# Kernel optimization log

Hardware: AMD Instinct MI355X
Metric: run time of the kernel (lower is better)

## Reference

```python
import jax, jax.numpy as jnp
import numpy as np

NUM_HEADS = 16
EPS = 1e-6
NEG_INF = -1e9


def layer_norm(x, scale, bias):
    m = jnp.mean(x, axis=-1, keepdims=True)
    v = jnp.mean(jnp.square(x - m), axis=-1, keepdims=True)
    return (x - m) * jax.lax.rsqrt(v + EPS) * scale + bias


def mha(x_q, x_kv, wq, wk, wv, wo, causal):
    B, Sq, D = x_q.shape
    Sk = x_kv.shape[1]
    H = NUM_HEADS
    Dh = D // H
    q = (x_q @ wq).reshape(B, Sq, H, Dh) * (1.0 / np.sqrt(Dh))
    k = (x_kv @ wk).reshape(B, Sk, H, Dh)
    v = (x_kv @ wv).reshape(B, Sk, H, Dh)
    scores = jnp.einsum('bqhf,bkhf->bhqk', q, k)  # [B,H,Sq,Sk]
    if causal:
        mask = jnp.tril(jnp.ones((Sq, Sk), dtype=bool))
        scores = jnp.where(mask, scores, NEG_INF)
    p = jax.nn.softmax(scores, axis=-1)
    o = jnp.einsum('bhqk,bkhf->bqhf', p, v).reshape(B, Sq, D)
    return o @ wo


def setup_inputs() -> dict:
    key = jax.random.key(0)
    ks = jax.random.split(key, 12)
    B, S, D, F = 2, 2048, 1024, 4096
    w = 0.02
    return {
        'targets': jax.random.normal(ks[0], (B, S, D), jnp.float32),
        'encoded': jax.random.normal(ks[1], (B, S, D), jnp.float32),
        'ln1_s': jnp.ones((D,), jnp.float32),
        'ln1_b': jnp.zeros((D,), jnp.float32),
        'sa_wq': jax.random.normal(ks[2], (D, D), jnp.float32) * w,
        'sa_wk': jax.random.normal(ks[3], (D, D), jnp.float32) * w,
        'sa_wv': jax.random.normal(ks[4], (D, D), jnp.float32) * w,
        'sa_wo': jax.random.normal(ks[5], (D, D), jnp.float32) * w,
        'ln2_s': jnp.ones((D,), jnp.float32),
        'ln2_b': jnp.zeros((D,), jnp.float32),
        'ca_wq': jax.random.normal(ks[6], (D, D), jnp.float32) * w,
        'ca_wk': jax.random.normal(ks[7], (D, D), jnp.float32) * w,
        'ca_wv': jax.random.normal(ks[8], (D, D), jnp.float32) * w,
        'ca_wo': jax.random.normal(ks[9], (D, D), jnp.float32) * w,
        'ln3_s': jnp.ones((D,), jnp.float32),
        'ln3_b': jnp.zeros((D,), jnp.float32),
        'mlp_w1': jax.random.normal(ks[10], (D, F), jnp.float32) * w,
        'mlp_b1': jnp.zeros((F,), jnp.float32),
        'mlp_w2': jax.random.normal(ks[11], (F, D), jnp.float32) * w,
        'mlp_b2': jnp.zeros((D,), jnp.float32),
    }


def reference(targets, encoded, ln1_s, ln1_b, sa_wq, sa_wk, sa_wv, sa_wo,
              ln2_s, ln2_b, ca_wq, ca_wk, ca_wv, ca_wo,
              ln3_s, ln3_b, mlp_w1, mlp_b1, mlp_w2, mlp_b2):
    # Pre-LN causal self-attention + residual
    x = layer_norm(targets, ln1_s, ln1_b)
    x = mha(x, x, sa_wq, sa_wk, sa_wv, sa_wo, causal=True)
    x = x + targets
    # Pre-LN cross-attention over encoder output + residual
    y = layer_norm(x, ln2_s, ln2_b)
    y = mha(y, encoded, ca_wq, ca_wk, ca_wv, ca_wo, causal=False)
    y = y + x
    # Pre-LN MLP + residual
    z = layer_norm(y, ln3_s, ln3_b)
    z = jax.nn.relu(z @ mlp_w1 + mlp_b1) @ mlp_w2 + mlp_b2
    return y + z
```

## Files before the change

kernel.cpp:

```cpp
#include <hip/hip_runtime.h>


#define DEV __device__ __forceinline__

typedef __attribute__((ext_vector_type(8))) _Float16 half8;
typedef __attribute__((ext_vector_type(4))) _Float16 half4;
typedef __attribute__((ext_vector_type(2))) _Float16 half2v;
typedef __attribute__((ext_vector_type(4))) float    f32x4;
typedef __attribute__((ext_vector_type(4))) unsigned int uint4v;

#define GLB(p) ((const __attribute__((address_space(1))) void*)(p))
#define LDS(p) ((__attribute__((address_space(3))) void*)(p))

DEV half2v pk(float a, float b) {
  return __builtin_bit_cast(half2v, __builtin_amdgcn_cvt_pkrtz(a, b));
}
DEV half4 pk4(float a, float b, float c, float d) {
  half2v lo = pk(a, b), hi = pk(c, d);
  half4 r; r.x = lo.x; r.y = lo.y; r.z = hi.x; r.w = hi.y;
  return r;
}

DEV float wave_sum_f(float v) {
  #pragma unroll
  for (int off = 32; off; off >>= 1) v += __shfl_xor(v, off);
  return v;
}

struct WtArgs { const float* w[8]; _Float16* wt[8]; };

__global__ __launch_bounds__(256) void wt_square(WtArgs a) {
  const float* w = a.w[blockIdx.z];
  _Float16* wt = a.wt[blockIdx.z];
  __shared__ float t[32][33];
  const int tx = threadIdx.x, ty = threadIdx.y;
  const int n0 = blockIdx.x * 32, k0 = blockIdx.y * 32;
  #pragma unroll
  for (int i = ty; i < 32; i += 8)
    t[i][tx] = w[(size_t)(k0 + i) * 1024 + n0 + tx];
  __syncthreads();
  #pragma unroll
  for (int i = ty; i < 32; i += 8)
    wt[(size_t)(n0 + i) * 1024 + k0 + tx] = (_Float16)t[tx][i];
}

__global__ __launch_bounds__(256) void wt_one(const float* __restrict__ w,
                                              _Float16* __restrict__ wt,
                                              int K, int N) {
  __shared__ float t[32][33];
  const int tx = threadIdx.x, ty = threadIdx.y;
  const int n0 = blockIdx.x * 32, k0 = blockIdx.y * 32;
  #pragma unroll
  for (int i = ty; i < 32; i += 8)
    t[i][tx] = w[(size_t)(k0 + i) * N + n0 + tx];
  __syncthreads();
  #pragma unroll
  for (int i = ty; i < 32; i += 8)
    wt[(size_t)(n0 + i) * K + k0 + tx] = (_Float16)t[tx][i];
}

__global__ __launch_bounds__(256) void cvt_f16(const float* __restrict__ in,
                                               _Float16* __restrict__ out) {
  const size_t i = ((size_t)blockIdx.x * 256 + threadIdx.x) * 4;
  const float4 v = *(const float4*)(in + i);
  *(half4*)(out + i) = pk4(v.x, v.y, v.z, v.w);
}

__global__ __launch_bounds__(256) void ln_kernel(const float* __restrict__ x,
                                                 const float* __restrict__ sc,
                                                 const float* __restrict__ bi,
                                                 _Float16* __restrict__ out) {
  const int row = blockIdx.x;
  const int t = threadIdx.x;
  const float4 v = ((const float4*)(x + (size_t)row * 1024))[t];
  float s  = v.x + v.y + v.z + v.w;
  float s2 = v.x * v.x + v.y * v.y + v.z * v.z + v.w * v.w;
  s = wave_sum_f(s); s2 = wave_sum_f(s2);
  __shared__ float red[8];
  const int lane = t & 63, wid = t >> 6;
  if (lane == 0) { red[wid] = s; red[4 + wid] = s2; }
  __syncthreads();
  s  = red[0] + red[1] + red[2] + red[3];
  s2 = red[4] + red[5] + red[6] + red[7];
  const float mean = s * (1.f / 1024.f);
  const float rstd = rsqrtf(s2 * (1.f / 1024.f) - mean * mean + 1e-6f);
  const float4 sv = ((const float4*)sc)[t];
  const float4 bv = ((const float4*)bi)[t];
  half4 o = pk4((v.x - mean) * rstd * sv.x + bv.x,
                (v.y - mean) * rstd * sv.y + bv.y,
                (v.z - mean) * rstd * sv.z + bv.z,
                (v.w - mean) * rstd * sv.w + bv.w);
  ((half4*)(out + (size_t)row * 1024))[t] = o;
}

template <int EPI, int BM, int BN, int BK>
__global__ __launch_bounds__(256)
void gemm_f16(const _Float16* __restrict__ A, const _Float16* __restrict__ Bt,
              void* __restrict__ Cout, const float* __restrict__ bias,
              const float* __restrict__ resid, int M, int N, int K,
              float scl, int sclCols, _Float16* __restrict__ vt, int vcol0) {
  constexpr int AM = BM / 32;
  constexpr int AN = BN / 32;
  constexpr int RA = BM * BK / 2048;
  constexpr int RB = BN * BK / 2048;
  constexpr int TPR = BK / 8;
  constexpr int RPR = 2048 / BK;
  constexpr int SWM = TPR - 1;
  constexpr int SH  = (TPR == 4) ? 1 : 0;
  __shared__ _Float16 As[2][BM * BK];
  __shared__ _Float16 Bs[2][BN * BK];
  const int tid = threadIdx.x;
  const int lane = tid & 63, wid = tid >> 6;
  const int wm = wid >> 1, wn = wid & 1;
  const int q = lane >> 4, m15 = lane & 15;

  const int nwg = gridDim.x * gridDim.y;
  const int bflat = blockIdx.x + gridDim.x * blockIdx.y;
  const int swz = (bflat & 7) * (nwg >> 3) + (bflat >> 3);
  const int bn = swz % gridDim.x;
  const int bm = swz / gridDim.x;

  const int trow = tid / TPR;
  const int tcolsw = ((tid % TPR) ^ ((trow >> SH) & SWM)) * 8;
  const _Float16* Ab = A + ((size_t)bm * BM + trow) * K + tcolsw;
  const _Float16* Bb = Bt + ((size_t)bn * BN + trow) * K + tcolsw;

  f32x4 acc[AM][AN] = {};

  auto stage = [&](int k0, int buf) {
    #pragma unroll
    for (int r = 0; r < RA; r++)
      __builtin_amdgcn_global_load_lds(GLB(Ab + (size_t)r * RPR * K + k0),
                                       LDS(&As[buf][r * 2048 + wid * 512]), 16, 0, 0);
    #pragma unroll
    for (int r = 0; r < RB; r++)
      __builtin_amdgcn_global_load_lds(GLB(Bb + (size_t)r * RPR * K + k0),
                                       LDS(&Bs[buf][r * 2048 + wid * 512]), 16, 0, 0);
  };

  stage(0, 0);
  const int nit = K / BK;
  for (int it = 0; it < nit; it++) {
    const int buf = it & 1;
    __syncthreads();
    if (it + 1 < nit) stage((it + 1) * BK, buf ^ 1);
    #pragma unroll
    for (int kk = 0; kk < BK / 32; kk++) {
      half8 af[AM], bf[AN];
      #pragma unroll
      for (int i = 0; i < AM; i++) {
        const int ra = wm * (BM / 2) + i * 16 + m15;
        af[i] = *(const half8*)&As[buf][ra * BK + (((kk * 4 + q) ^ ((ra >> SH) & SWM)) << 3)];
      }
      #pragma unroll
      for (int i = 0; i < AN; i++) {
        const int rb = wn * (BN / 2) + i * 16 + m15;
        bf[i] = *(const half8*)&Bs[buf][rb * BK + (((kk * 4 + q) ^ ((rb >> SH) & SWM)) << 3)];
      }
      #pragma unroll
      for (int mi = 0; mi < AM; mi++)
        #pragma unroll
        for (int ni = 0; ni < AN; ni++)
          acc[mi][ni] = __builtin_amdgcn_mfma_f32_16x16x32_f16(af[mi], bf[ni],
                                                               acc[mi][ni], 0, 0, 0);
    }
  }

  const int rowbase = bm * BM + wm * (BM / 2);
  const int colbase = bn * BN + wn * (BN / 2);
  #pragma unroll
  for (int ni = 0; ni < AN; ni++) {
    const int col = colbase + ni * 16 + m15;
    float bv = 0.f;
    if (EPI == 2 || EPI == 4) bv = bias[col];
    const float cs = (EPI == 1 || EPI == 5) ? (col < sclCols ? scl : 1.f) : 1.f;
    if (EPI == 5 && col >= vcol0) {
      const int d = col & 63, hh = (col >> 6) & 15;
      #pragma unroll
      for (int mi = 0; mi < AM; mi++) {
        const int row = rowbase + mi * 16 + q * 4;
        const int bb = row >> 11, ss = row & 2047;
        half4 ov = pk4(acc[mi][ni][0], acc[mi][ni][1],
                       acc[mi][ni][2], acc[mi][ni][3]);
        *(half4*)(vt + ((size_t)(bb * 16 + hh) * 64 + d) * 2048 + ss) = ov;
      }
      continue;
    }
    #pragma unroll
    for (int mi = 0; mi < AM; mi++) {
      #pragma unroll
      for (int r = 0; r < 4; r++) {
        const int row = rowbase + mi * 16 + q * 4 + r;
        const size_t idx = (size_t)row * N + col;
        float v = acc[mi][ni][r];
        if (EPI == 1 || EPI == 5) {
          ((_Float16*)Cout)[idx] = (_Float16)(v * cs);
        } else if (EPI == 2) {
          v += bv; v = v > 0.f ? v : 0.f;
          ((_Float16*)Cout)[idx] = (_Float16)v;
        } else if (EPI == 3) {
          ((float*)Cout)[idx] = v + resid[idx];
        } else {
          ((float*)Cout)[idx] = v + bv + resid[idx];
        }
      }
    }
  }
}

__global__ __launch_bounds__(512, 4)
void flash_attn(const _Float16* __restrict__ Q, int qs,
                const _Float16* __restrict__ Kp, int ks,
                const _Float16* __restrict__ Vt,
                _Float16* __restrict__ Opart, float* __restrict__ Lpart,
                int S, int Sk, int causal) {
  __shared__ _Float16 Ks[2][64 * 64];
  __shared__ _Float16 Vs[2][64 * 64];
  const int tid = threadIdx.x;
  const int lane = tid & 63, wid = tid >> 6;
  const int quad = lane >> 4, c15 = lane & 15;

  const int gx = gridDim.x;
  const int lid = blockIdx.x + gx * (blockIdx.y + 16 * blockIdx.z);
  const int xcd = lid & 7, slot = lid >> 3;
  const int bh = xcd * 4 + (slot / gx);
  const int qs2 = slot % gx;
  const int h = bh & 15, b = bh >> 4;
  int qb = qs2 >> 1;
  const int split = qs2 & 1;
  const int NQB = gx >> 1;
  if (causal) qb = (qb & 1) ? (NQB - 1 - (qb >> 1)) : (qb >> 1);
  const int qw0 = qb * 256 + wid * 32;

  half8 qf[2][2];
  #pragma unroll
  for (int nt = 0; nt < 2; nt++)
    #pragma unroll
    for (int kk = 0; kk < 2; kk++)
      qf[nt][kk] = *(const half8*)(Q + (size_t)(b * S + qw0 + nt * 16 + c15) * qs +
                                   h * 64 + kk * 32 + quad * 8);

  f32x4 oacc[4][2];
  #pragma unroll
  for (int i = 0; i < 4; i++)
    #pragma unroll
    for (int j = 0; j < 2; j++)
      oacc[i][j] = (f32x4){0.f, 0.f, 0.f, 0.f};
  float lpart[2] = {0.f, 0.f};

  const int ntF = causal ? (4 * qb + 4) : (Sk >> 6);
  const _Float16* Kg = Kp + (size_t)b * Sk * ks + h * 64;
  const _Float16* Vg = Vt + (size_t)(b * 16 + h) * 64 * Sk;

  const int srow = tid >> 3;
  const int ssw = (((tid & 7) ^ (srow & 7)) << 3);
  auto stage = [&](int jb, int buf) {
    __builtin_amdgcn_global_load_lds(
        GLB(Kg + (size_t)(jb + srow) * ks + ssw),
        LDS(&Ks[buf][(wid * 8) * 64]), 16, 0, 0);
    __builtin_amdgcn_global_load_lds(
        GLB(Vg + (size_t)srow * Sk + jb + ssw),
        LDS(&Vs[buf][(wid * 8) * 64]), 16, 0, 0);
  };

  const int t0 = split;
  stage(t0 << 6, 0);
  __syncthreads();

  const int rsw = c15 & 7;
  const int ck0 = ((quad ^ rsw) << 3);
  const int ck1 = (((quad ^ 4) ^ rsw) << 3);

  int cur = 0;
  for (int t = t0; t < ntF; t += 2) {
    const int jb = t << 6;
    if (t + 2 < ntF) stage((t + 2) << 6, cur ^ 1);

    if (!(causal && jb > qw0 + 31)) {
      f32x4 s[4][2];
      __builtin_amdgcn_s_setprio(1);
      #pragma unroll
      for (int mt = 0; mt < 4; mt++) {
        const half8 kf0 = *(const half8*)&Ks[cur][(mt * 16 + c15) * 64 + ck0];
        const half8 kf1 = *(const half8*)&Ks[cur][(mt * 16 + c15) * 64 + ck1];
        #pragma unroll
        for (int nt = 0; nt < 2; nt++) {
          f32x4 z = {0.f, 0.f, 0.f, 0.f};
          z = __builtin_amdgcn_mfma_f32_16x16x32_f16(kf0, qf[nt][0], z, 0, 0, 0);
          z = __builtin_amdgcn_mfma_f32_16x16x32_f16(kf1, qf[nt][1], z, 0, 0, 0);
          s[mt][nt] = z;
        }
      }
      __builtin_amdgcn_s_setprio(0);

      if (causal && jb + 63 > qw0) {
        #pragma unroll
        for (int mt = 0; mt < 4; mt++)
          #pragma unroll
          for (int nt = 0; nt < 2; nt++) {
            const int qglob = qw0 + nt * 16 + c15;
            #pragma unroll
            for (int rr = 0; rr < 4; rr++) {
              const int kglob = jb + mt * 16 + quad * 4 + rr;
              if (kglob > qglob) s[mt][nt][rr] = -1e30f;
            }
          }
      }

      unsigned int pkd[4][2][2];
      #pragma unroll
      for (int nt = 0; nt < 2; nt++) {
        float psum = 0.f;
        #pragma unroll
        for (int mt = 0; mt < 4; mt++) {
          #pragma unroll
          for (int rr = 0; rr < 4; rr++) {
            const float p = __builtin_amdgcn_exp2f(s[mt][nt][rr]);
            s[mt][nt][rr] = p;
            psum += p;
          }
          pkd[mt][nt][0] = __builtin_bit_cast(unsigned int,
                             pk(s[mt][nt][0], s[mt][nt][1]));
          pkd[mt][nt][1] = __builtin_bit_cast(unsigned int,
                             pk(s[mt][nt][2], s[mt][nt][3]));
        }
        lpart[nt] += psum;
      }

      half8 pb[2][2];
      #pragma unroll
      for (int kk = 0; kk < 2; kk++)
        #pragma unroll
        for (int nt = 0; nt < 2; nt++) {
          unsigned int w[4];
          #pragma unroll
          for (int jd = 0; jd < 4; jd++) {
            const int src = ((quad & 1) * 2 + (jd >> 1)) * 16 + c15;
            const unsigned int xs = __shfl(pkd[2 * kk][nt][jd & 1], src);
            const unsigned int ys = __shfl(pkd[2 * kk + 1][nt][jd & 1], src);
            w[jd] = (quad & 2) ? ys : xs;
          }
          uint4v u = {w[0], w[1], w[2], w[3]};
          pb[kk][nt] = __builtin_bit_cast(half8, u);
        }

      __builtin_amdgcn_s_setprio(1);
      #pragma unroll
      for (int mtd = 0; mtd < 4; mtd++) {
        const half8 vf0 = *(const half8*)&Vs[cur][(mtd * 16 + c15) * 64 + ck0];
        const half8 vf1 = *(const half8*)&Vs[cur][(mtd * 16 + c15) * 64 + ck1];
        #pragma unroll
        for (int nt = 0; nt < 2; nt++) {
          oacc[mtd][nt] = __builtin_amdgcn_mfma_f32_16x16x32_f16(vf0, pb[0][nt],
                                                                 oacc[mtd][nt], 0, 0, 0);
          oacc[mtd][nt] = __builtin_amdgcn_mfma_f32_16x16x32_f16(vf1, pb[1][nt],
                                                                 oacc[mtd][nt], 0, 0, 0);
        }
      }
      __builtin_amdgcn_s_setprio(0);
    }

    __syncthreads();
    cur ^= 1;
  }

  _Float16* Ob = Opart + (size_t)split * ((size_t)2 * S * 1024) +
                 (size_t)b * S * 1024;
  #pragma unroll
  for (int nt = 0; nt < 2; nt++) {
    float l = lpart[nt];
    l += __shfl_xor(l, 16);
    l += __shfl_xor(l, 32);
    const int qrow = qw0 + nt * 16 + c15;
    if (quad == 0)
      Lpart[((size_t)(split * 2 + b) * 16 + h) * S + qrow] = l;
    #pragma unroll
    for (int mtd = 0; mtd < 4; mtd++) {
      half4 ov = pk4(oacc[mtd][nt][0], oacc[mtd][nt][1],
                     oacc[mtd][nt][2], oacc[mtd][nt][3]);
      *(half4*)(Ob + (size_t)qrow * 1024 + h * 64 + mtd * 16 + quad * 4) = ov;
    }
  }
}

__global__ __launch_bounds__(256)
void attn_combine(const _Float16* __restrict__ Op, const float* __restrict__ Lp,
                  _Float16* __restrict__ O) {
  const int row = blockIdx.x, tid = threadIdx.x;
  const int col = tid << 2, h = tid >> 4;
  const int b = row >> 11, sq = row & 2047;
  const float la = Lp[((size_t)(b * 16 + h)) * 2048 + sq];
  const float lb = Lp[((size_t)((b + 2) * 16 + h)) * 2048 + sq];
  const float linv = 1.f / (la + lb);
  const half4 pa = *(const half4*)(Op + (size_t)row * 1024 + col);
  const half4 pb = *(const half4*)(Op + ((size_t)4096 + row) * 1024 + col);
  half4 o = pk4(((float)pa.x + (float)pb.x) * linv,
                ((float)pa.y + (float)pb.y) * linv,
                ((float)pa.z + (float)pb.z) * linv,
                ((float)pa.w + (float)pb.w) * linv);
  *(half4*)(O + (size_t)row * 1024 + col) = o;
}

extern "C" void kernel_launch(void* const* d_in, const int* in_sizes, int n_in,
                              void* d_out, int out_size, void* d_ws, size_t ws_size,
                              hipStream_t stream) {
  const float* targets = (const float*)d_in[0];
  const float* encoded = (const float*)d_in[1];
  const float* ln1_s = (const float*)d_in[2];
  const float* ln1_b = (const float*)d_in[3];
  const float* sa_wq = (const float*)d_in[4];
  const float* sa_wk = (const float*)d_in[5];
  const float* sa_wv = (const float*)d_in[6];
  const float* sa_wo = (const float*)d_in[7];
  const float* ln2_s = (const float*)d_in[8];
  const float* ln2_b = (const float*)d_in[9];
  const float* ca_wq = (const float*)d_in[10];
  const float* ca_wk = (const float*)d_in[11];
  const float* ca_wv = (const float*)d_in[12];
  const float* ca_wo = (const float*)d_in[13];
  const float* ln3_s = (const float*)d_in[14];
  const float* ln3_b = (const float*)d_in[15];
  const float* mlp_w1 = (const float*)d_in[16];
  const float* mlp_b1 = (const float*)d_in[17];
  const float* mlp_w2 = (const float*)d_in[18];
  const float* mlp_b2 = (const float*)d_in[19];

  const int B = 2, S = 2048, D = 1024, F = 4096, M = B * S;
  const size_t MB = 1024ull * 1024ull;
  const float QSCALE = 0.125f * 1.44269504f;
  char* ws = (char*)d_ws;
  _Float16* wsq   = (_Float16*)(ws);
  _Float16* w1t   = (_Float16*)(ws + 16 * MB);
  _Float16* w2t   = (_Float16*)(ws + 24 * MB);
  _Float16* Abf   = (_Float16*)(ws + 32 * MB);
  _Float16* encbf = (_Float16*)(ws + 40 * MB);
  _Float16* QKV   = (_Float16*)(ws + 48 * MB);
  _Float16* Qcb   = (_Float16*)(ws + 48 * MB);
  _Float16* KVb   = (_Float16*)(ws + 56 * MB);
  _Float16* h1    = (_Float16*)(ws + 48 * MB);
  float*    Lbuf  = (float*)(ws + 72 * MB);
  _Float16* Vtb   = (_Float16*)(ws + 80 * MB);
  _Float16* Aob   = (_Float16*)(ws + 88 * MB);
  float*    xres  = (float*)(ws + 96 * MB);
  float*    yres  = (float*)(ws + 112 * MB);
  _Float16* Opart = (_Float16*)(ws + 112 * MB);

  {
    WtArgs wa;
    const float* sw[8] = {sa_wq, sa_wk, sa_wv, sa_wo, ca_wq, ca_wk, ca_wv, ca_wo};
    for (int i = 0; i < 8; i++) { wa.w[i] = sw[i]; wa.wt[i] = wsq + (size_t)i * D * D; }
    wt_square<<<dim3(32, 32, 8), dim3(32, 8), 0, stream>>>(wa);
  }
  wt_one<<<dim3(F / 32, D / 32), dim3(32, 8), 0, stream>>>(mlp_w1, w1t, D, F);
  wt_one<<<dim3(D / 32, F / 32), dim3(32, 8), 0, stream>>>(mlp_w2, w2t, F, D);
  cvt_f16<<<(M * D) / 1024, 256, 0, stream>>>(encoded, encbf);

  const dim3 gA(2 * (S / 256), 16, B);

  ln_kernel<<<M, 256, 0, stream>>>(targets, ln1_s, ln1_b, Abf);
  gemm_f16<5, 128, 128, 32><<<dim3(3072 / 128, M / 128), 256, 0, stream>>>(
      Abf, wsq, QKV, nullptr, nullptr, M, 3072, D, QSCALE, 1024, Vtb, 2048);
  flash_attn<<<gA, 512, 0, stream>>>(QKV, 3072, QKV + 1024, 3072, Vtb,
                                     Opart, Lbuf, S, S, 1);
  attn_combine<<<M, 256, 0, stream>>>(Opart, Lbuf, Aob);
  gemm_f16<3, 64, 64, 64><<<dim3(1024 / 64, M / 64), 256, 0, stream>>>(
      Aob, wsq + 3ull * D * D, xres, nullptr, targets, M, D, D, 1.f, 0, nullptr, 0);

  ln_kernel<<<M, 256, 0, stream>>>(xres, ln2_s, ln2_b, Abf);
  gemm_f16<1, 64, 64, 64><<<dim3(1024 / 64, M / 64), 256, 0, stream>>>(
      Abf, wsq + 4ull * D * D, Qcb, nullptr, nullptr, M, D, D, QSCALE, 1024, nullptr, 0);
  gemm_f16<5, 64, 128, 32><<<dim3(2048 / 128, M / 64), 256, 0, stream>>>(
      encbf, wsq + 5ull * D * D, KVb, nullptr, nullptr, M, 2048, D, 1.f, 0, Vtb, 1024);
  flash_attn<<<gA, 512, 0, stream>>>(Qcb, 1024, KVb, 2048, Vtb,
                                     Opart, Lbuf, S, S, 0);
  attn_combine<<<M, 256, 0, stream>>>(Opart, Lbuf, Aob);
  gemm_f16<3, 64, 64, 64><<<dim3(1024 / 64, M / 64), 256, 0, stream>>>(
      Aob, wsq + 7ull * D * D, yres, nullptr, xres, M, D, D, 1.f, 0, nullptr, 0);

  ln_kernel<<<M, 256, 0, stream>>>(yres, ln3_s, ln3_b, Abf);
  gemm_f16<2, 128, 128, 32><<<dim3(F / 128, M / 128), 256, 0, stream>>>(
      Abf, w1t, h1, mlp_b1, nullptr, M, F, D, 1.f, 0, nullptr, 0);
  gemm_f16<4, 64, 64, 64><<<dim3(1024 / 64, M / 64), 256, 0, stream>>>(
      h1, w2t, (float*)d_out, mlp_b2, yres, M, D, F, 1.f, 0, nullptr, 0);

  (void)in_sizes; (void)n_in; (void)out_size; (void)ws_size;
}
```

Baseline: 516.9 us.

## Split flash attention KV range four ways and combine four partials

```diff
diff --git a/kernel.cpp b/kernel.cpp
--- a/kernel.cpp
+++ b/kernel.cpp
@@ -26,6 +26,8 @@
   for (int off = 32; off; off >>= 1) v += __shfl_xor(v, off);
   return v;
 }
+
+struct OpPtrs { _Float16* p[4]; };
 
 struct WtArgs { const float* w[8]; _Float16* wt[8]; };
 
@@ -208,11 +210,11 @@
   }
 }
 
-__global__ __launch_bounds__(512, 4)
+__global__ __launch_bounds__(512, 8)
 void flash_attn(const _Float16* __restrict__ Q, int qs,
                 const _Float16* __restrict__ Kp, int ks,
                 const _Float16* __restrict__ Vt,
-                _Float16* __restrict__ Opart, float* __restrict__ Lpart,
+                OpPtrs Pp, float* __restrict__ Lpart,
                 int S, int Sk, int causal) {
   __shared__ _Float16 Ks[2][64 * 64];
   __shared__ _Float16 Vs[2][64 * 64];
@@ -226,9 +228,9 @@
   const int bh = xcd * 4 + (slot / gx);
   const int qs2 = slot % gx;
   const int h = bh & 15, b = bh >> 4;
-  int qb = qs2 >> 1;
-  const int split = qs2 & 1;
-  const int NQB = gx >> 1;
+  int qb = qs2 >> 2;
+  const int split = qs2 & 3;
+  const int NQB = gx >> 2;
   if (causal) qb = (qb & 1) ? (NQB - 1 - (qb >> 1)) : (qb >> 1);
   const int qw0 = qb * 256 + wid * 32;
 
@@ -272,9 +274,9 @@
   const int ck1 = (((quad ^ 4) ^ rsw) << 3);
 
   int cur = 0;
-  for (int t = t0; t < ntF; t += 2) {
+  for (int t = t0; t < ntF; t += 4) {
     const int jb = t << 6;
-    if (t + 2 < ntF) stage((t + 2) << 6, cur ^ 1);
+    if (t + 4 < ntF) stage((t + 4) << 6, cur ^ 1);
 
     if (!(causal && jb > qw0 + 31)) {
       f32x4 s[4][2];
@@ -364,8 +366,7 @@
     cur ^= 1;
   }
 
-  _Float16* Ob = Opart + (size_t)split * ((size_t)2 * S * 1024) +
-                 (size_t)b * S * 1024;
+  _Float16* Ob = Pp.p[split] + (size_t)b * S * 1024;
   #pragma unroll
   for (int nt = 0; nt < 2; nt++) {
     float l = lpart[nt];
@@ -384,20 +385,22 @@
 }
 
 __global__ __launch_bounds__(256)
-void attn_combine(const _Float16* __restrict__ Op, const float* __restrict__ Lp,
-                  _Float16* __restrict__ O) {
+void attn_combine(OpPtrs Pp, const float* Lp, _Float16* O) {
   const int row = blockIdx.x, tid = threadIdx.x;
   const int col = tid << 2, h = tid >> 4;
   const int b = row >> 11, sq = row & 2047;
-  const float la = Lp[((size_t)(b * 16 + h)) * 2048 + sq];
-  const float lb = Lp[((size_t)((b + 2) * 16 + h)) * 2048 + sq];
-  const float linv = 1.f / (la + lb);
-  const half4 pa = *(const half4*)(Op + (size_t)row * 1024 + col);
-  const half4 pb = *(const half4*)(Op + ((size_t)4096 + row) * 1024 + col);
-  half4 o = pk4(((float)pa.x + (float)pb.x) * linv,
-                ((float)pa.y + (float)pb.y) * linv,
-                ((float)pa.z + (float)pb.z) * linv,
-                ((float)pa.w + (float)pb.w) * linv);
+  float l = 0.f;
+  #pragma unroll
+  for (int s2 = 0; s2 < 4; s2++)
+    l += Lp[((size_t)(s2 * 2 + b) * 16 + h) * 2048 + sq];
+  const float linv = 1.f / l;
+  float ax = 0.f, ay = 0.f, az = 0.f, aw = 0.f;
+  #pragma unroll
+  for (int s2 = 0; s2 < 4; s2++) {
+    const half4 p = *(const half4*)(Pp.p[s2] + (size_t)row * 1024 + col);
+    ax += (float)p.x; ay += (float)p.y; az += (float)p.z; aw += (float)p.w;
+  }
+  half4 o = pk4(ax * linv, ay * linv, az * linv, aw * linv);
   *(half4*)(O + (size_t)row * 1024 + col) = o;
 }
 
@@ -443,7 +446,11 @@
   _Float16* Aob   = (_Float16*)(ws + 88 * MB);
   float*    xres  = (float*)(ws + 96 * MB);
   float*    yres  = (float*)(ws + 112 * MB);
-  _Float16* Opart = (_Float16*)(ws + 112 * MB);
+  OpPtrs op;
+  op.p[0] = (_Float16*)(ws + 112 * MB);
+  op.p[1] = (_Float16*)(ws + 120 * MB);
+  op.p[2] = Abf;
+  op.p[3] = Aob;
 
   {
     WtArgs wa;
@@ -455,14 +462,14 @@
   wt_one<<<dim3(D / 32, F / 32), dim3(32, 8), 0, stream>>>(mlp_w2, w2t, F, D);
   cvt_f16<<<(M * D) / 1024, 256, 0, stream>>>(encoded, encbf);
 
-  const dim3 gA(2 * (S / 256), 16, B);
+  const dim3 gA(4 * (S / 256), 16, B);
 
   ln_kernel<<<M, 256, 0, stream>>>(targets, ln1_s, ln1_b, Abf);
   gemm_f16<5, 128, 128, 32><<<dim3(3072 / 128, M / 128), 256, 0, stream>>>(
       Abf, wsq, QKV, nullptr, nullptr, M, 3072, D, QSCALE, 1024, Vtb, 2048);
   flash_attn<<<gA, 512, 0, stream>>>(QKV, 3072, QKV + 1024, 3072, Vtb,
-                                     Opart, Lbuf, S, S, 1);
-  attn_combine<<<M, 256, 0, stream>>>(Opart, Lbuf, Aob);
+                                     op, Lbuf, S, S, 1);
+  attn_combine<<<M, 256, 0, stream>>>(op, Lbuf, Aob);
   gemm_f16<3, 64, 64, 64><<<dim3(1024 / 64, M / 64), 256, 0, stream>>>(
       Aob, wsq + 3ull * D * D, xres, nullptr, targets, M, D, D, 1.f, 0, nullptr, 0);
 
@@ -472,8 +479,8 @@
   gemm_f16<5, 64, 128, 32><<<dim3(2048 / 128, M / 64), 256, 0, stream>>>(
       encbf, wsq + 5ull * D * D, KVb, nullptr, nullptr, M, 2048, D, 1.f, 0, Vtb, 1024);
   flash_attn<<<gA, 512, 0, stream>>>(Qcb, 1024, KVb, 2048, Vtb,
-                                     Opart, Lbuf, S, S, 0);
-  attn_combine<<<M, 256, 0, stream>>>(Opart, Lbuf, Aob);
+                                     op, Lbuf, S, S, 0);
+  attn_combine<<<M, 256, 0, stream>>>(op, Lbuf, Aob);
   gemm_f16<3, 64, 64, 64><<<dim3(1024 / 64, M / 64), 256, 0, stream>>>(
       Aob, wsq + 7ull * D * D, yres, nullptr, xres, M, D, D, 1.f, 0, nullptr, 0);
 
```

Measured after the change: 926.8 us. 79.3% more time.
